# Performance work log

Hardware: AMD Instinct MI355X
Metric: run time of the kernel (lower is better)

## Reference

```python
import jax, jax.numpy as jnp
import numpy as np

B, N, ADA, L, D_OUT, C_T, N_DIS = 8, 2048, 16, 64, 16, 4, 8
H = L // D_OUT  # 4 heads emulated via split/cat on the batch dim


def setup_inputs() -> dict:
    key = jax.random.key(0)
    ks = jax.random.split(key, 12)
    f = lambda i, shape, s=1.0: jax.random.normal(ks[i], shape, dtype=jnp.float32) * s
    return dict(
        c=f(0, (B, N, L)),
        c_condition=f(1, (B, C_T)),
        c_disease=f(2, (B, N_DIS)),
        state=f(3, (B, N, L)),
        emb_normal=f(4, (N, ADA)),                 # nn.Parameter embeddings_normal
        W_q1=f(5, (C_T, L), 0.1), b_q1=jnp.zeros((L,), jnp.float32),
        W_qr1=f(6, (1, L), 0.1),  b_qr1=jnp.zeros((L,), jnp.float32),
        W_q2=f(7, (L, L), 0.1),   b_q2=jnp.zeros((L,), jnp.float32),
        W_qr2=f(8, (L, L), 0.1),  b_qr2=jnp.zeros((L,), jnp.float32),
        Wp_gcn=f(9, (ADA, 2, L, L), 0.1),          # adaptive weight pool (cheb_k=2)
        bp_gcn=f(10, (ADA, L), 0.1),               # adaptive bias pool
    )


def _to_heads(t):
    # torch.cat(torch.split(t, D_OUT, dim=-1), dim=0): [B,N,H*d] -> [H*B,N,d]
    return jnp.concatenate(jnp.split(t, H, axis=-1), axis=0)


def _from_heads(t):
    # inverse: [H*B,N,d] -> [B,N,H*d]
    return jnp.concatenate(jnp.split(t, H, axis=0), axis=-1)


def _anode_gcn(x, E, Wp, bp):
    # adaptive GCN (AGCRN-style AVWGCN): supports=[I, softmax(relu(E E^T))]
    A = jax.nn.softmax(jax.nn.relu(E @ E.T), axis=1)          # [N,N]
    xg = jnp.stack([x, jnp.einsum('nm,bmc->bnc', A, x)], 1)   # [B,2,N,C]
    Wn = jnp.einsum('nd,dkio->nkio', E, Wp)                   # per-node weights
    bn = E @ bp                                               # [N,L]
    return jnp.einsum('bkni,nkio->bno', xg, Wn) + bn


def reference(c, c_condition, c_disease, state, emb_normal,
              W_q1, b_q1, W_qr1, b_qr1, W_q2, b_q2, W_qr2, b_qr2,
              Wp_gcn, bp_gcn):
    # gated query path
    Qt = jax.nn.sigmoid(c_condition[:, None, :] @ W_q1 + b_q1)        # [B,1,L]
    Qt = jnp.tanh((Qt * c) @ W_q2 + b_q2)                             # [B,N,L]
    # disease loop vectorized: sum_n sigmoid(Linear(c_disease[:, n:n+1]))
    qr = jax.nn.sigmoid(c_disease[:, :, None] * W_qr1[0] + b_qr1)     # [B,D,L]
    qr = qr.sum(axis=1, keepdims=True)                                # [B,1,L]
    qr = Qt + jnp.tanh((qr * c) @ W_qr2 + b_qr2)                      # [B,N,L]
    qr_h = _to_heads(qr)  # computed in the original but unused in output

    theta = _to_heads(state)                                          # [HB,N,d]
    ct = jnp.tanh(_anode_gcn(c, emb_normal, Wp_gcn, bp_gcn))          # [B,N,L]
    ct = _to_heads(ct)                                                # [HB,N,d]

    attn = jnp.einsum('bnd,bmd->bnm', theta, theta) / jnp.sqrt(jnp.float32(D_OUT))
    attn = jax.nn.softmax(attn, axis=-1)                              # [HB,N,N]
    x = -jnp.einsum('bnm,bmd->bnd', attn, ct)                         # [HB,N,d]
    return _from_heads(x)                                             # [B,N,L]
```

## Files before the change

### kernel.cpp

```cpp
#include <hip/hip_runtime.h>
#include <hip/hip_bf16.h>

#define NN 2048
#define BB 8
#define LL 64
#define ADA 16
#define DH 16
#define HB 32
#define KT 2048

typedef __attribute__((ext_vector_type(4))) short bf16x4;
typedef __attribute__((ext_vector_type(4))) float f32x4;
typedef __attribute__((ext_vector_type(8))) unsigned short ushort8v;
typedef _Float16 half_t;
typedef __attribute__((ext_vector_type(2))) _Float16 halfx2;
typedef __attribute__((ext_vector_type(4))) _Float16 halfx4;
typedef __attribute__((ext_vector_type(8))) _Float16 halfx8;

#if defined(__HIP_DEVICE_COMPILE__)
#if __has_builtin(__builtin_amdgcn_mfma_f32_16x16x16bf16_1k)
#define MFMA16(a, b, c) __builtin_amdgcn_mfma_f32_16x16x16bf16_1k(a, b, c, 0, 0, 0)
#elif __has_builtin(__builtin_amdgcn_mfma_f32_16x16x16_bf16)
#define MFMA16(a, b, c) __builtin_amdgcn_mfma_f32_16x16x16_bf16(a, b, c, 0, 0, 0)
#else
#error "no 16x16x16 bf16 mfma builtin on device"
#endif
#if __has_builtin(__builtin_amdgcn_mfma_f32_16x16x16f16)
#define MFMA16H(a, b, c) __builtin_amdgcn_mfma_f32_16x16x16f16(a, b, c, 0, 0, 0)
#elif __has_builtin(__builtin_amdgcn_mfma_f32_16x16x16_f16)
#define MFMA16H(a, b, c) __builtin_amdgcn_mfma_f32_16x16x16_f16(a, b, c, 0, 0, 0)
#else
#error "no 16x16x16 f16 mfma builtin on device"
#endif
#if __has_builtin(__builtin_amdgcn_exp2f)
#define EXP2F(x) __builtin_amdgcn_exp2f(x)
#else
#define EXP2F(x) exp2f(x)
#endif
#else
#define MFMA16(a, b, c) (c)
#define MFMA16H(a, b, c) (c)
#define EXP2F(x) exp2f(x)
#endif

__device__ inline halfx2 cvt_pk2(float a, float b) {
#if defined(__HIP_DEVICE_COMPILE__) && __has_builtin(__builtin_amdgcn_cvt_pkrtz)
  auto r = __builtin_amdgcn_cvt_pkrtz(a, b);
  return __builtin_bit_cast(halfx2, r);
#else
  halfx2 r;
  r[0] = (_Float16)a;
  r[1] = (_Float16)b;
  return r;
#endif
}

__device__ inline unsigned short f2bf(float x) {
  __hip_bfloat16 h = __float2bfloat16(x);
  return *reinterpret_cast<unsigned short*>(&h);
}
__device__ inline float tanh_fast(float v) {
  return 1.f - 2.f / (__expf(2.f * v) + 1.f);
}

__global__ __launch_bounds__(256) void k_rowsoftmax(const float* __restrict__ E,
                                                    unsigned short* __restrict__ A16) {
  __shared__ float row[4][NN];
  __shared__ float red[4][256];
  const int n = blockIdx.x * 4;
  const int t = threadIdx.x;
  float4 e[4][4];
#pragma unroll
  for (int r = 0; r < 4; ++r) {
    const float4* Er = (const float4*)(E + (size_t)(n + r) * ADA);
#pragma unroll
    for (int j = 0; j < 4; ++j) e[r][j] = Er[j];
  }
  float l[4] = {0.f, 0.f, 0.f, 0.f};
  for (int m = t; m < NN; m += 256) {
    const float4* Em = (const float4*)(E + (size_t)m * ADA);
    float4 ev[4];
#pragma unroll
    for (int j = 0; j < 4; ++j) ev[j] = Em[j];
#pragma unroll
    for (int r = 0; r < 4; ++r) {
      float s = 0.f;
#pragma unroll
      for (int j = 0; j < 4; ++j) {
        s = fmaf(e[r][j].x, ev[j].x, s);
        s = fmaf(e[r][j].y, ev[j].y, s);
        s = fmaf(e[r][j].z, ev[j].z, s);
        s = fmaf(e[r][j].w, ev[j].w, s);
      }
      float p = __expf(fmaxf(s, 0.f) - 20.f);
      row[r][m] = p;
      l[r] += p;
    }
  }
#pragma unroll
  for (int r = 0; r < 4; ++r) red[r][t] = l[r];
  __syncthreads();
  for (int off = 128; off > 0; off >>= 1) {
    if (t < off) {
#pragma unroll
      for (int r = 0; r < 4; ++r) red[r][t] += red[r][t + off];
    }
    __syncthreads();
  }
  float inv[4];
#pragma unroll
  for (int r = 0; r < 4; ++r) inv[r] = 1.f / red[r][0];
  for (int m = t; m < NN; m += 256) {
#pragma unroll
    for (int r = 0; r < 4; ++r)
      A16[(size_t)(n + r) * NN + m] = f2bf(row[r][m] * inv[r]);
  }
}

__global__ __launch_bounds__(256) void k_prep_c(const float* __restrict__ c,
                                                unsigned short* __restrict__ cT16) {
  __shared__ float ld[64][68];
  const int m0 = blockIdx.x * 64;
  const int b = blockIdx.y;
  const int t = threadIdx.x;
  {
    const int r = t & 63, cq = t >> 6;
    const float* cp = c + ((size_t)b * NN + m0 + r) * LL + cq * 16;
#pragma unroll
    for (int u = 0; u < 4; ++u)
      *(float4*)&ld[r][cq * 16 + 4 * u] = *(const float4*)(cp + 4 * u);
  }
  __syncthreads();
  const int o = t & 63, mq = t >> 6;
  unsigned short outv[16];
#pragma unroll
  for (int v = 0; v < 16; ++v) outv[v] = f2bf(ld[mq * 16 + v][o]);
  unsigned short* op = cT16 + ((size_t)b * LL + o) * NN + m0 + mq * 16;
  *(ushort8v*)op = *(const ushort8v*)&outv[0];
  *(ushort8v*)(op + 8) = *(const ushort8v*)&outv[8];
}

__global__ __launch_bounds__(256) void k_prep_w(const float* __restrict__ Wp,
                                                half_t* __restrict__ WpT) {
  __shared__ float ld[64][68];
  const int k0 = blockIdx.x * 64;
  const int t = threadIdx.x;
  {
    const int r = t & 63, cq = t >> 6;
    const float* wp = Wp + (size_t)(k0 + r) * LL + cq * 16;
#pragma unroll
    for (int u = 0; u < 4; ++u)
      *(float4*)&ld[r][cq * 16 + 4 * u] = *(const float4*)(wp + 4 * u);
  }
  __syncthreads();
  const int o = t & 63, kq = t >> 6;
  halfx8 h0, h1;
#pragma unroll
  for (int v = 0; v < 8; ++v) {
    h0[v] = (half_t)ld[kq * 16 + v][o];
    h1[v] = (half_t)ld[kq * 16 + 8 + v][o];
  }
  half_t* op = WpT + (size_t)o * KT + k0 + kq * 16;
  *(halfx8*)op = h0;
  *(halfx8*)(op + 8) = h1;
}

__global__ __launch_bounds__(256) void k_gemm1(const unsigned short* __restrict__ A16,
                                               const unsigned short* __restrict__ cT16,
                                               float* __restrict__ cg0,
                                               float* __restrict__ cg1) {
  __shared__ unsigned short sA[64][72];
  __shared__ unsigned short sB[64][72];
  const int t = threadIdx.x;
  const int n0 = blockIdx.x * 64;
  const int b = blockIdx.y;
  const int kh = blockIdx.z;
  const int wv = t >> 6, lane = t & 63;
  const int lr = lane & 15, lg = lane >> 4;
  const unsigned short* cb = cT16 + (size_t)b * LL * NN;
  const int sr = t >> 2, sc = (t & 3) * 16;
  f32x4 acc[4];
#pragma unroll
  for (int ot = 0; ot < 4; ++ot) acc[ot] = (f32x4){0.f, 0.f, 0.f, 0.f};

  for (int k0 = kh * (NN / 2); k0 < (kh + 1) * (NN / 2); k0 += 64) {
    __syncthreads();
    {
      const unsigned short* ga = A16 + (size_t)(n0 + sr) * NN + k0 + sc;
      *(ushort8v*)&sA[sr][sc] = *(const ushort8v*)ga;
      *(ushort8v*)&sA[sr][sc + 8] = *(const ushort8v*)(ga + 8);
      const unsigned short* gb = cb + (size_t)sr * NN + k0 + sc;
      *(ushort8v*)&sB[sr][sc] = *(const ushort8v*)gb;
      *(ushort8v*)&sB[sr][sc + 8] = *(const ushort8v*)(gb + 8);
    }
    __syncthreads();
#pragma unroll
    for (int ks = 0; ks < 4; ++ks) {
      bf16x4 a = *(const bf16x4*)&sA[16 * wv + lr][ks * 16 + 4 * lg];
#pragma unroll
      for (int ot = 0; ot < 4; ++ot) {
        bf16x4 bq = *(const bf16x4*)&sB[ot * 16 + lr][ks * 16 + 4 * lg];
        acc[ot] = MFMA16(a, bq, acc[ot]);
      }
    }
  }
  float* outp = (kh ? cg1 : cg0) + ((size_t)b * NN + n0 + 16 * wv) * LL;
#pragma unroll
  for (int ot = 0; ot < 4; ++ot)
#pragma unroll
    for (int reg = 0; reg < 4; ++reg)
      outp[(size_t)(4 * lg + reg) * LL + ot * 16 + lr] = acc[ot][reg];
}

__global__ __launch_bounds__(256) void k_gcn3(const float* __restrict__ E,
                                              const half_t* __restrict__ WpT,
                                              const float* __restrict__ bp,
                                              const float* __restrict__ c,
                                              const float* __restrict__ cg0,
                                              const float* __restrict__ cg1,
                                              float* __restrict__ ctp0,
                                              float* __restrict__ ctp1) {
  __shared__ half_t sW[64][136];
  __shared__ float sE[64][17];
  __shared__ float sbp[16][64];
  const int t = threadIdx.x;
  const int n0 = blockIdx.x * 64;
  const int b = blockIdx.y;
  const int dh = blockIdx.z;
  const int wv = t >> 6, lane = t & 63;
  const int lr = lane & 15, lg = lane >> 4;
  {
    const int r = t >> 2, dq = (t & 3) * 4;
    float4 ev = *(const float4*)(E + (size_t)(n0 + r) * ADA + dq);
    sE[r][dq + 0] = ev.x; sE[r][dq + 1] = ev.y;
    sE[r][dq + 2] = ev.z; sE[r][dq + 3] = ev.w;
    const int bi = t * 4;
    *(float4*)&sbp[bi >> 6][bi & 63] = *(const float4*)(bp + bi);
  }
  float xr[8][4];
  {
    const size_t rbase = ((size_t)b * NN + n0 + 16 * wv + lr) * LL;
#pragma unroll
    for (int q = 0; q < 4; ++q) {
      float4 v = *(const float4*)(c + rbase + q * 16 + 4 * lg);
      xr[q][0] = v.x; xr[q][1] = v.y; xr[q][2] = v.z; xr[q][3] = v.w;
    }
#pragma unroll
    for (int q = 0; q < 4; ++q) {
      float4 a = *(const float4*)(cg0 + rbase + q * 16 + 4 * lg);
      float4 b2 = *(const float4*)(cg1 + rbase + q * 16 + 4 * lg);
      xr[4 + q][0] = a.x + b2.x; xr[4 + q][1] = a.y + b2.y;
      xr[4 + q][2] = a.z + b2.z; xr[4 + q][3] = a.w + b2.w;
    }
  }
  __syncthreads();
  f32x4 acc[4];
  if (dh == 0) {
#pragma unroll
    for (int ot = 0; ot < 4; ++ot) {
      f32x4 s = (f32x4){0.f, 0.f, 0.f, 0.f};
#pragma unroll
      for (int d = 0; d < ADA; ++d) {
        const float bpv = sbp[d][ot * 16 + lr];
#pragma unroll
        for (int reg = 0; reg < 4; ++reg)
          s[reg] = fmaf(sE[16 * wv + 4 * lg + reg][d], bpv, s[reg]);
      }
      acc[ot] = s;
    }
  } else {
#pragma unroll
    for (int ot = 0; ot < 4; ++ot) acc[ot] = (f32x4){0.f, 0.f, 0.f, 0.f};
  }
  const int so = t >> 2, sq = t & 3;
  halfx8 wreg[4];
  {
    const half_t* p = WpT + (size_t)so * KT + (size_t)(dh * 8) * 128;
#pragma unroll
    for (int u = 0; u < 4; ++u) wreg[u] = *(const halfx8*)(p + (sq + 4 * u) * 8);
  }
  for (int dd = 0; dd < 8; ++dd) {
    __syncthreads();
#pragma unroll
    for (int u = 0; u < 4; ++u) *(halfx8*)&sW[so][(sq + 4 * u) * 8] = wreg[u];
    __syncthreads();
    if (dd < 7) {
      const half_t* p = WpT + (size_t)so * KT + (size_t)(dh * 8 + dd + 1) * 128;
#pragma unroll
      for (int u = 0; u < 4; ++u) wreg[u] = *(const halfx8*)(p + (sq + 4 * u) * 8);
    }
    const float e = sE[16 * wv + lr][dh * 8 + dd];
    halfx4 af[8];
#pragma unroll
    for (int kt = 0; kt < 8; ++kt)
#pragma unroll
      for (int j = 0; j < 4; ++j) af[kt][j] = (half_t)(e * xr[kt][j]);
#pragma unroll
    for (int kt = 0; kt < 8; ++kt) {
#pragma unroll
      for (int ot = 0; ot < 4; ++ot) {
        halfx4 bq = *(const halfx4*)&sW[ot * 16 + lr][kt * 16 + 4 * lg];
        acc[ot] = MFMA16H(af[kt], bq, acc[ot]);
      }
    }
  }
  float* op = (dh ? ctp1 : ctp0) + ((size_t)b * NN + n0 + 16 * wv) * LL;
#pragma unroll
  for (int ot = 0; ot < 4; ++ot)
#pragma unroll
    for (int reg = 0; reg < 4; ++reg)
      op[(size_t)(4 * lg + reg) * LL + ot * 16 + lr] = acc[ot][reg];
}

__global__ __launch_bounds__(256) void k_prep(const float* __restrict__ state,
                                              const float* __restrict__ ctp0,
                                              const float* __restrict__ ctp1,
                                              half_t* __restrict__ th16h,
                                              half_t* __restrict__ thq16h,
                                              half_t* __restrict__ vt16h) {
  __shared__ half_t vt[16][68];
  const int hb = blockIdx.x;
  const int h = hb >> 3, b = hb & 7;
  const int n0 = blockIdx.y * 64;
  const int t = threadIdx.x;
  const int r = t >> 2, dq = t & 3;
  const float QS = 0.25f * 1.4426950408889634f;
  const float* sp = state + ((size_t)b * NN + n0 + r) * LL + h * DH + 4 * dq;
  float4 sv = *(const float4*)sp;
  halfx4 tk;
  tk[0] = (half_t)sv.x; tk[1] = (half_t)sv.y; tk[2] = (half_t)sv.z; tk[3] = (half_t)sv.w;
  *(halfx4*)(th16h + ((size_t)hb * NN + n0 + r) * DH + 4 * dq) = tk;
  halfx4 tq;
  tq[0] = (half_t)(QS * sv.x); tq[1] = (half_t)(QS * sv.y);
  tq[2] = (half_t)(QS * sv.z); tq[3] = (half_t)(QS * sv.w);
  *(halfx4*)(thq16h + ((size_t)hb * NN + n0 + r) * DH + 4 * dq) = tq;
  const size_t cidx = ((size_t)b * NN + n0 + r) * LL + h * DH + 4 * dq;
  float4 p0 = *(const float4*)(ctp0 + cidx);
  float4 p1 = *(const float4*)(ctp1 + cidx);
  vt[4 * dq + 0][r] = (half_t)tanh_fast(p0.x + p1.x);
  vt[4 * dq + 1][r] = (half_t)tanh_fast(p0.y + p1.y);
  vt[4 * dq + 2][r] = (half_t)tanh_fast(p0.z + p1.z);
  vt[4 * dq + 3][r] = (half_t)tanh_fast(p0.w + p1.w);
  __syncthreads();
  const int d = t >> 4, mq = t & 15;
  halfx4 o;
  o[0] = vt[d][4 * mq + 0]; o[1] = vt[d][4 * mq + 1];
  o[2] = vt[d][4 * mq + 2]; o[3] = vt[d][4 * mq + 3];
  *(halfx4*)(vt16h + ((size_t)hb * DH + d) * NN + n0 + 4 * mq) = o;
}

__global__ __launch_bounds__(512, 4) void k_attn5(const half_t* __restrict__ th16h,
                                                  const half_t* __restrict__ thq16h,
                                                  const half_t* __restrict__ vt16h,
                                                  float* __restrict__ out) {
  __shared__ float sred[8][8][16][16];
  float* dfl = &sred[0][0][0][0];
  const int hb = blockIdx.x;
  const int h = hb >> 3, b = hb & 7;
  const int wv = threadIdx.x >> 6, lane = threadIdx.x & 63;
  const int q0 = blockIdx.y * 128;
  const int lr = lane & 15, lg = lane >> 4;
  const half_t* th = th16h + (size_t)hb * NN * DH;
  const half_t* thq = thq16h + (size_t)hb * NN * DH;
  const half_t* vrow = vt16h + ((size_t)hb * DH + lr) * NN;
  halfx4 qf[8];
#pragma unroll
  for (int f = 0; f < 8; ++f)
    qf[f] = *(const halfx4*)(thq + (size_t)(q0 + 16 * f + lr) * DH + 4 * lg);
  const float SH = 8.f * 1.4426950408889634f;
  const f32x4 shiftv = {-SH, -SH, -SH, -SH};
  f32x4 acc[8];
  float den[8];
#pragma unroll
  for (int f = 0; f < 8; ++f) { acc[f] = (f32x4){0.f, 0.f, 0.f, 0.f}; den[f] = 0.f; }

  const int mb = wv * (NN / 8);
  halfx4 kf = *(const halfx4*)(th + (size_t)(mb + lr) * DH + 4 * lg);
  halfx4 vf = *(const halfx4*)(vrow + mb + 4 * lg);
  for (int mt = 0; mt < NN / 128; ++mt) {
    halfx4 kf_n = kf, vf_n = vf;
    if (mt < NN / 128 - 1) {
      const int mn = mb + (mt + 1) * 16;
      kf_n = *(const halfx4*)(th + (size_t)(mn + lr) * DH + 4 * lg);
      vf_n = *(const halfx4*)(vrow + mn + 4 * lg);
    }
#pragma unroll
    for (int f = 0; f < 8; ++f) {
      f32x4 s = MFMA16H(kf, qf[f], shiftv);
      float p0 = EXP2F(s[0]), p1 = EXP2F(s[1]), p2 = EXP2F(s[2]), p3 = EXP2F(s[3]);
      den[f] += (p0 + p1) + (p2 + p3);
      halfx2 lo = cvt_pk2(p0, p1), hi = cvt_pk2(p2, p3);
      halfx4 pf;
      pf[0] = lo[0]; pf[1] = lo[1]; pf[2] = hi[0]; pf[3] = hi[1];
      acc[f] = MFMA16H(pf, vf, acc[f]);
    }
    kf = kf_n; vf = vf_n;
  }
#pragma unroll
  for (int f = 0; f < 8; ++f) {
    den[f] += __shfl_xor(den[f], 16);
    den[f] += __shfl_xor(den[f], 32);
  }
  if (lane < 16) {
#pragma unroll
    for (int f = 0; f < 8; ++f) dfl[(wv * 8 + f) * 16 + lane] = den[f];
  }
  __syncthreads();
  const int t = threadIdx.x;
  const int fo = t >> 6, ro = (t >> 2) & 15, duo = (t & 3) * 4;
  float ds = 0.f;
#pragma unroll
  for (int w = 0; w < 8; ++w) ds += dfl[(w * 8 + fo) * 16 + ro];
  __syncthreads();
#pragma unroll
  for (int f = 0; f < 8; ++f) {
#pragma unroll
    for (int reg = 0; reg < 4; ++reg) sred[wv][f][4 * lg + reg][lr] = acc[f][reg];
  }
  __syncthreads();
  float4 ns = make_float4(0.f, 0.f, 0.f, 0.f);
#pragma unroll
  for (int w = 0; w < 8; ++w) {
    float4 v = *(const float4*)&sred[w][fo][ro][duo];
    ns.x += v.x; ns.y += v.y; ns.z += v.z; ns.w += v.w;
  }
  const float inv = -1.f / ds;
  float4 o = make_float4(ns.x * inv, ns.y * inv, ns.z * inv, ns.w * inv);
  *(float4*)(out + ((size_t)b * NN + q0 + 16 * fo + ro) * LL + h * DH + duo) = o;
}

extern "C" void kernel_launch(void* const* d_in, const int* in_sizes, int n_in,
                              void* d_out, int out_size, void* d_ws, size_t ws_size,
                              hipStream_t stream) {
  const float* c = (const float*)d_in[0];
  const float* state = (const float*)d_in[3];
  const float* E = (const float*)d_in[4];
  const float* Wp = (const float*)d_in[13];
  const float* bp = (const float*)d_in[14];
  float* out = (float*)d_out;

  unsigned short* A16 = (unsigned short*)d_ws;
  unsigned short* cT16 = A16 + (size_t)NN * NN;
  half_t* WpT = (half_t*)(cT16 + (size_t)BB * LL * NN);
  float* cg0 = (float*)(WpT + (size_t)LL * KT);
  float* cg1 = cg0 + (size_t)BB * NN * LL;
  float* ctp0 = cg1 + (size_t)BB * NN * LL;
  float* ctp1 = ctp0 + (size_t)BB * NN * LL;
  half_t* th16h = (half_t*)(ctp1 + (size_t)BB * NN * LL);
  half_t* thq16h = th16h + (size_t)HB * NN * DH;
  half_t* vt16h = thq16h + (size_t)HB * NN * DH;

  k_rowsoftmax<<<NN / 4, 256, 0, stream>>>(E, A16);
  k_prep_c<<<dim3(NN / 64, BB), 256, 0, stream>>>(c, cT16);
  k_prep_w<<<KT / 64, 256, 0, stream>>>(Wp, WpT);
  k_gemm1<<<dim3(NN / 64, BB, 2), 256, 0, stream>>>(A16, cT16, cg0, cg1);
  k_gcn3<<<dim3(NN / 64, BB, 2), 256, 0, stream>>>(E, WpT, bp, c, cg0, cg1, ctp0, ctp1);
  k_prep<<<dim3(HB, NN / 64), 256, 0, stream>>>(state, ctp0, ctp1, th16h, thq16h, vt16h);
  k_attn5<<<dim3(HB, NN / 128), 512, 0, stream>>>(th16h, thq16h, vt16h, out);
}
```

Before: 76.41 us.

## Merge prep kernels into one launch and fuse tanh/value transpose into GCN

Merges the row-softmax, c-transpose, weight-transpose and state/theta conversion into a single multi-role kernel dispatched on block index, cutting launches. The GCN kernel now splits over output halves instead of the ADA dimension, so each block covers all 16 embedding dims for 32 outputs. It applies tanh and writes the transposed fp16 value tensor directly, which removes the ctp0/ctp1 fp32 intermediates and the separate prep kernel. In exchange each GCN block does a longer serial loop with more barriers, and the merged prep kernel has uneven block roles.

```diff
diff --git a/kernel.cpp b/kernel.cpp
--- a/kernel.cpp
+++ b/kernel.cpp
@@ -63,106 +63,131 @@
   return 1.f - 2.f / (__expf(2.f * v) + 1.f);
 }
 
-__global__ __launch_bounds__(256) void k_rowsoftmax(const float* __restrict__ E,
-                                                    unsigned short* __restrict__ A16) {
-  __shared__ float row[4][NN];
-  __shared__ float red[4][256];
-  const int n = blockIdx.x * 4;
+__global__ __launch_bounds__(256) void k_preps(const float* __restrict__ E,
+                                               const float* __restrict__ c,
+                                               const float* __restrict__ state,
+                                               const float* __restrict__ Wp,
+                                               unsigned short* __restrict__ A16,
+                                               unsigned short* __restrict__ cT16,
+                                               half_t* __restrict__ WpT,
+                                               half_t* __restrict__ th16h,
+                                               half_t* __restrict__ thq16h) {
+  __shared__ float sbuf[4 * 2304];
+  const int id = blockIdx.x;
   const int t = threadIdx.x;
-  float4 e[4][4];
-#pragma unroll
-  for (int r = 0; r < 4; ++r) {
-    const float4* Er = (const float4*)(E + (size_t)(n + r) * ADA);
-#pragma unroll
-    for (int j = 0; j < 4; ++j) e[r][j] = Er[j];
-  }
-  float l[4] = {0.f, 0.f, 0.f, 0.f};
-  for (int m = t; m < NN; m += 256) {
-    const float4* Em = (const float4*)(E + (size_t)m * ADA);
-    float4 ev[4];
-#pragma unroll
-    for (int j = 0; j < 4; ++j) ev[j] = Em[j];
+  if (id < 512) {
+    float(*row)[NN] = (float(*)[NN])sbuf;
+    float(*red)[256] = (float(*)[256])(sbuf + 4 * NN);
+    const int n = id * 4;
+    float4 e[4][4];
 #pragma unroll
     for (int r = 0; r < 4; ++r) {
-      float s = 0.f;
-#pragma unroll
-      for (int j = 0; j < 4; ++j) {
-        s = fmaf(e[r][j].x, ev[j].x, s);
-        s = fmaf(e[r][j].y, ev[j].y, s);
-        s = fmaf(e[r][j].z, ev[j].z, s);
-        s = fmaf(e[r][j].w, ev[j].w, s);
+      const float4* Er = (const float4*)(E + (size_t)(n + r) * ADA);
+#pragma unroll
+      for (int j = 0; j < 4; ++j) e[r][j] = Er[j];
+    }
+    float l[4] = {0.f, 0.f, 0.f, 0.f};
+    for (int m = t; m < NN; m += 256) {
+      const float4* Em = (const float4*)(E + (size_t)m * ADA);
+      float4 ev[4];
+#pragma unroll
+      for (int j = 0; j < 4; ++j) ev[j] = Em[j];
+#pragma unroll
+      for (int r = 0; r < 4; ++r) {
+        float s = 0.f;
+#pragma unroll
+        for (int j = 0; j < 4; ++j) {
+          s = fmaf(e[r][j].x, ev[j].x, s);
+          s = fmaf(e[r][j].y, ev[j].y, s);
+          s = fmaf(e[r][j].z, ev[j].z, s);
+          s = fmaf(e[r][j].w, ev[j].w, s);
+        }
+        float p = __expf(fmaxf(s, 0.f) - 20.f);
+        row[r][m] = p;
+        l[r] += p;
       }
-      float p = __expf(fmaxf(s, 0.f) - 20.f);
-      row[r][m] = p;
-      l[r] += p;
-    }
-  }
-#pragma unroll
-  for (int r = 0; r < 4; ++r) red[r][t] = l[r];
-  __syncthreads();
-  for (int off = 128; off > 0; off >>= 1) {
-    if (t < off) {
-#pragma unroll
-      for (int r = 0; r < 4; ++r) red[r][t] += red[r][t + off];
-    }
-    __syncthreads();
-  }
-  float inv[4];
-#pragma unroll
-  for (int r = 0; r < 4; ++r) inv[r] = 1.f / red[r][0];
-  for (int m = t; m < NN; m += 256) {
-#pragma unroll
-    for (int r = 0; r < 4; ++r)
-      A16[(size_t)(n + r) * NN + m] = f2bf(row[r][m] * inv[r]);
-  }
-}
-
-__global__ __launch_bounds__(256) void k_prep_c(const float* __restrict__ c,
-                                                unsigned short* __restrict__ cT16) {
-  __shared__ float ld[64][68];
-  const int m0 = blockIdx.x * 64;
-  const int b = blockIdx.y;
-  const int t = threadIdx.x;
-  {
-    const int r = t & 63, cq = t >> 6;
-    const float* cp = c + ((size_t)b * NN + m0 + r) * LL + cq * 16;
-#pragma unroll
-    for (int u = 0; u < 4; ++u)
-      *(float4*)&ld[r][cq * 16 + 4 * u] = *(const float4*)(cp + 4 * u);
-  }
-  __syncthreads();
-  const int o = t & 63, mq = t >> 6;
-  unsigned short outv[16];
-#pragma unroll
-  for (int v = 0; v < 16; ++v) outv[v] = f2bf(ld[mq * 16 + v][o]);
-  unsigned short* op = cT16 + ((size_t)b * LL + o) * NN + m0 + mq * 16;
-  *(ushort8v*)op = *(const ushort8v*)&outv[0];
-  *(ushort8v*)(op + 8) = *(const ushort8v*)&outv[8];
-}
-
-__global__ __launch_bounds__(256) void k_prep_w(const float* __restrict__ Wp,
-                                                half_t* __restrict__ WpT) {
-  __shared__ float ld[64][68];
-  const int k0 = blockIdx.x * 64;
-  const int t = threadIdx.x;
-  {
-    const int r = t & 63, cq = t >> 6;
-    const float* wp = Wp + (size_t)(k0 + r) * LL + cq * 16;
-#pragma unroll
-    for (int u = 0; u < 4; ++u)
-      *(float4*)&ld[r][cq * 16 + 4 * u] = *(const float4*)(wp + 4 * u);
-  }
-  __syncthreads();
-  const int o = t & 63, kq = t >> 6;
-  halfx8 h0, h1;
-#pragma unroll
-  for (int v = 0; v < 8; ++v) {
-    h0[v] = (half_t)ld[kq * 16 + v][o];
-    h1[v] = (half_t)ld[kq * 16 + 8 + v][o];
-  }
-  half_t* op = WpT + (size_t)o * KT + k0 + kq * 16;
-  *(halfx8*)op = h0;
-  *(halfx8*)(op + 8) = h1;
+    }
+#pragma unroll
+    for (int r = 0; r < 4; ++r) red[r][t] = l[r];
+    __syncthreads();
+    for (int off = 128; off > 0; off >>= 1) {
+      if (t < off) {
+#pragma unroll
+        for (int r = 0; r < 4; ++r) red[r][t] += red[r][t + off];
+      }
+      __syncthreads();
+    }
+    float inv[4];
+#pragma unroll
+    for (int r = 0; r < 4; ++r) inv[r] = 1.f / red[r][0];
+    for (int m = t; m < NN; m += 256) {
+#pragma unroll
+      for (int r = 0; r < 4; ++r)
+        A16[(size_t)(n + r) * NN + m] = f2bf(row[r][m] * inv[r]);
+    }
+  } else if (id < 768) {
+    float(*ld)[68] = (float(*)[68])sbuf;
+    const int idx = id - 512;
+    const int m0 = (idx & 31) * 64;
+    const int b = idx >> 5;
+    {
+      const int r = t & 63, cq = t >> 6;
+      const float* cp = c + ((size_t)b * NN + m0 + r) * LL + cq * 16;
+#pragma unroll
+      for (int u = 0; u < 4; ++u)
+        *(float4*)&ld[r][cq * 16 + 4 * u] = *(const float4*)(cp + 4 * u);
+    }
+    __syncthreads();
+    const int o = t & 63, mq = t >> 6;
+    unsigned short outv[16];
+#pragma unroll
+    for (int v = 0; v < 16; ++v) outv[v] = f2bf(ld[mq * 16 + v][o]);
+    unsigned short* op = cT16 + ((size_t)b * LL + o) * NN + m0 + mq * 16;
+    *(ushort8v*)op = *(const ushort8v*)&outv[0];
+    *(ushort8v*)(op + 8) = *(const ushort8v*)&outv[8];
+  } else if (id < 800) {
+    float(*ld)[68] = (float(*)[68])sbuf;
+    const int k0 = (id - 768) * 64;
+    {
+      const int r = t & 63, cq = t >> 6;
+      const float* wp = Wp + (size_t)(k0 + r) * LL + cq * 16;
+#pragma unroll
+      for (int u = 0; u < 4; ++u)
+        *(float4*)&ld[r][cq * 16 + 4 * u] = *(const float4*)(wp + 4 * u);
+    }
+    __syncthreads();
+    const int o = t & 63, kq = t >> 6;
+    halfx8 h0, h1;
+#pragma unroll
+    for (int v = 0; v < 8; ++v) {
+      h0[v] = (half_t)ld[kq * 16 + v][o];
+      h1[v] = (half_t)ld[kq * 16 + 8 + v][o];
+    }
+    half_t* op = WpT + (size_t)o * KT + k0 + kq * 16;
+    *(halfx8*)op = h0;
+    *(halfx8*)(op + 8) = h1;
+  } else {
+    const int idx = id - 800;
+    const int n0 = (idx & 31) * 64;
+    const int b = idx >> 5;
+    const int r = t >> 2, h = t & 3;
+    const float QS = 0.25f * 1.4426950408889634f;
+    const float* sp = state + ((size_t)b * NN + n0 + r) * LL + h * DH;
+    half_t tk[16], tq[16];
+#pragma unroll
+    for (int u = 0; u < 4; ++u) {
+      float4 sv = *(const float4*)(sp + 4 * u);
+      tk[4 * u + 0] = (half_t)sv.x; tk[4 * u + 1] = (half_t)sv.y;
+      tk[4 * u + 2] = (half_t)sv.z; tk[4 * u + 3] = (half_t)sv.w;
+      tq[4 * u + 0] = (half_t)(QS * sv.x); tq[4 * u + 1] = (half_t)(QS * sv.y);
+      tq[4 * u + 2] = (half_t)(QS * sv.z); tq[4 * u + 3] = (half_t)(QS * sv.w);
+    }
+    const size_t base = ((size_t)(h * 8 + b) * NN + n0 + r) * DH;
+    *(halfx8*)(th16h + base) = *(const halfx8*)&tk[0];
+    *(halfx8*)(th16h + base + 8) = *(const halfx8*)&tk[8];
+    *(halfx8*)(thq16h + base) = *(const halfx8*)&tq[0];
+    *(halfx8*)(thq16h + base + 8) = *(const halfx8*)&tq[8];
+  }
 }
 
 __global__ __launch_bounds__(256) void k_gemm1(const unsigned short* __restrict__ A16,
@@ -212,21 +237,20 @@
       outp[(size_t)(4 * lg + reg) * LL + ot * 16 + lr] = acc[ot][reg];
 }
 
-__global__ __launch_bounds__(256) void k_gcn3(const float* __restrict__ E,
+__global__ __launch_bounds__(256) void k_gcn4(const float* __restrict__ E,
                                               const half_t* __restrict__ WpT,
                                               const float* __restrict__ bp,
                                               const float* __restrict__ c,
                                               const float* __restrict__ cg0,
                                               const float* __restrict__ cg1,
-                                              float* __restrict__ ctp0,
-                                              float* __restrict__ ctp1) {
-  __shared__ half_t sW[64][136];
+                                              half_t* __restrict__ vt16h) {
+  __shared__ half_t sW[32][136];
   __shared__ float sE[64][17];
-  __shared__ float sbp[16][64];
+  __shared__ float sbp[16][32];
   const int t = threadIdx.x;
   const int n0 = blockIdx.x * 64;
   const int b = blockIdx.y;
-  const int dh = blockIdx.z;
+  const int oh = blockIdx.z;
   const int wv = t >> 6, lane = t & 63;
   const int lr = lane & 15, lg = lane >> 4;
   {
@@ -234,8 +258,10 @@
     float4 ev = *(const float4*)(E + (size_t)(n0 + r) * ADA + dq);
     sE[r][dq + 0] = ev.x; sE[r][dq + 1] = ev.y;
     sE[r][dq + 2] = ev.z; sE[r][dq + 3] = ev.w;
-    const int bi = t * 4;
-    *(float4*)&sbp[bi >> 6][bi & 63] = *(const float4*)(bp + bi);
+    const int d = t >> 4, o2 = (t & 15) * 2;
+    float2 bv = *(const float2*)(bp + d * LL + oh * 32 + o2);
+    sbp[d][o2] = bv.x;
+    sbp[d][o2 + 1] = bv.y;
   }
   float xr[8][4];
   {
@@ -254,99 +280,59 @@
     }
   }
   __syncthreads();
-  f32x4 acc[4];
-  if (dh == 0) {
-#pragma unroll
-    for (int ot = 0; ot < 4; ++ot) {
-      f32x4 s = (f32x4){0.f, 0.f, 0.f, 0.f};
-#pragma unroll
-      for (int d = 0; d < ADA; ++d) {
-        const float bpv = sbp[d][ot * 16 + lr];
-#pragma unroll
-        for (int reg = 0; reg < 4; ++reg)
-          s[reg] = fmaf(sE[16 * wv + 4 * lg + reg][d], bpv, s[reg]);
+  f32x4 acc[2];
+#pragma unroll
+  for (int ot2 = 0; ot2 < 2; ++ot2) {
+    f32x4 s = (f32x4){0.f, 0.f, 0.f, 0.f};
+#pragma unroll
+    for (int d = 0; d < ADA; ++d) {
+      const float bpv = sbp[d][ot2 * 16 + lr];
+#pragma unroll
+      for (int reg = 0; reg < 4; ++reg)
+        s[reg] = fmaf(sE[16 * wv + 4 * lg + reg][d], bpv, s[reg]);
+    }
+    acc[ot2] = s;
+  }
+  const int so = t >> 3, sq = t & 7;
+  halfx8 wreg[2];
+  {
+    const half_t* p = WpT + (size_t)(oh * 32 + so) * KT + sq * 16;
+    wreg[0] = *(const halfx8*)p;
+    wreg[1] = *(const halfx8*)(p + 8);
+  }
+  for (int dd = 0; dd < ADA; ++dd) {
+    __syncthreads();
+    *(halfx8*)&sW[so][sq * 16] = wreg[0];
+    *(halfx8*)&sW[so][sq * 16 + 8] = wreg[1];
+    __syncthreads();
+    if (dd < ADA - 1) {
+      const half_t* p = WpT + (size_t)(oh * 32 + so) * KT + (dd + 1) * 128 + sq * 16;
+      wreg[0] = *(const halfx8*)p;
+      wreg[1] = *(const halfx8*)(p + 8);
+    }
+    const float e = sE[16 * wv + lr][dd];
+    halfx4 af[8];
+#pragma unroll
+    for (int kt = 0; kt < 8; ++kt)
+#pragma unroll
+      for (int j = 0; j < 4; ++j) af[kt][j] = (half_t)(e * xr[kt][j]);
+#pragma unroll
+    for (int kt = 0; kt < 8; ++kt) {
+#pragma unroll
+      for (int ot2 = 0; ot2 < 2; ++ot2) {
+        halfx4 bq = *(const halfx4*)&sW[ot2 * 16 + lr][kt * 16 + 4 * lg];
+        acc[ot2] = MFMA16H(af[kt], bq, acc[ot2]);
       }
-      acc[ot] = s;
-    }
-  } else {
-#pragma unroll
-    for (int ot = 0; ot < 4; ++ot) acc[ot] = (f32x4){0.f, 0.f, 0.f, 0.f};
-  }
-  const int so = t >> 2, sq = t & 3;
-  halfx8 wreg[4];
-  {
-    const half_t* p = WpT + (size_t)so * KT + (size_t)(dh * 8) * 128;
-#pragma unroll
-    for (int u = 0; u < 4; ++u) wreg[u] = *(const halfx8*)(p + (sq + 4 * u) * 8);
-  }
-  for (int dd = 0; dd < 8; ++dd) {
-    __syncthreads();
-#pragma unroll
-    for (int u = 0; u < 4; ++u) *(halfx8*)&sW[so][(sq + 4 * u) * 8] = wreg[u];
-    __syncthreads();
-    if (dd < 7) {
-      const half_t* p = WpT + (size_t)so * KT + (size_t)(dh * 8 + dd + 1) * 128;
-#pragma unroll
-      for (int u = 0; u < 4; ++u) wreg[u] = *(const halfx8*)(p + (sq + 4 * u) * 8);
-    }
-    const float e = sE[16 * wv + lr][dh * 8 + dd];
-    halfx4 af[8];
-#pragma unroll
-    for (int kt = 0; kt < 8; ++kt)
-#pragma unroll
-      for (int j = 0; j < 4; ++j) af[kt][j] = (half_t)(e * xr[kt][j]);
-#pragma unroll
-    for (int kt = 0; kt < 8; ++kt) {
-#pragma unroll
-      for (int ot = 0; ot < 4; ++ot) {
-        halfx4 bq = *(const halfx4*)&sW[ot * 16 + lr][kt * 16 + 4 * lg];
-        acc[ot] = MFMA16H(af[kt], bq, acc[ot]);
-      }
-    }
-  }
-  float* op = (dh ? ctp1 : ctp0) + ((size_t)b * NN + n0 + 16 * wv) * LL;
-#pragma unroll
-  for (int ot = 0; ot < 4; ++ot)
-#pragma unroll
-    for (int reg = 0; reg < 4; ++reg)
-      op[(size_t)(4 * lg + reg) * LL + ot * 16 + lr] = acc[ot][reg];
-}
-
-__global__ __launch_bounds__(256) void k_prep(const float* __restrict__ state,
-                                              const float* __restrict__ ctp0,
-                                              const float* __restrict__ ctp1,
-                                              half_t* __restrict__ th16h,
-                                              half_t* __restrict__ thq16h,
-                                              half_t* __restrict__ vt16h) {
-  __shared__ half_t vt[16][68];
-  const int hb = blockIdx.x;
-  const int h = hb >> 3, b = hb & 7;
-  const int n0 = blockIdx.y * 64;
-  const int t = threadIdx.x;
-  const int r = t >> 2, dq = t & 3;
-  const float QS = 0.25f * 1.4426950408889634f;
-  const float* sp = state + ((size_t)b * NN + n0 + r) * LL + h * DH + 4 * dq;
-  float4 sv = *(const float4*)sp;
-  halfx4 tk;
-  tk[0] = (half_t)sv.x; tk[1] = (half_t)sv.y; tk[2] = (half_t)sv.z; tk[3] = (half_t)sv.w;
-  *(halfx4*)(th16h + ((size_t)hb * NN + n0 + r) * DH + 4 * dq) = tk;
-  halfx4 tq;
-  tq[0] = (half_t)(QS * sv.x); tq[1] = (half_t)(QS * sv.y);
-  tq[2] = (half_t)(QS * sv.z); tq[3] = (half_t)(QS * sv.w);
-  *(halfx4*)(thq16h + ((size_t)hb * NN + n0 + r) * DH + 4 * dq) = tq;
-  const size_t cidx = ((size_t)b * NN + n0 + r) * LL + h * DH + 4 * dq;
-  float4 p0 = *(const float4*)(ctp0 + cidx);
-  float4 p1 = *(const float4*)(ctp1 + cidx);
-  vt[4 * dq + 0][r] = (half_t)tanh_fast(p0.x + p1.x);
-  vt[4 * dq + 1][r] = (half_t)tanh_fast(p0.y + p1.y);
-  vt[4 * dq + 2][r] = (half_t)tanh_fast(p0.z + p1.z);
-  vt[4 * dq + 3][r] = (half_t)tanh_fast(p0.w + p1.w);
-  __syncthreads();
-  const int d = t >> 4, mq = t & 15;
-  halfx4 o;
-  o[0] = vt[d][4 * mq + 0]; o[1] = vt[d][4 * mq + 1];
-  o[2] = vt[d][4 * mq + 2]; o[3] = vt[d][4 * mq + 3];
-  *(halfx4*)(vt16h + ((size_t)hb * DH + d) * NN + n0 + 4 * mq) = o;
+    }
+  }
+#pragma unroll
+  for (int ot2 = 0; ot2 < 2; ++ot2) {
+    const int h = oh * 2 + ot2;
+    halfx4 o4;
+#pragma unroll
+    for (int reg = 0; reg < 4; ++reg) o4[reg] = (half_t)tanh_fast(acc[ot2][reg]);
+    *(halfx4*)(vt16h + ((size_t)(h * 8 + b) * DH + lr) * NN + n0 + 16 * wv + 4 * lg) = o4;
+  }
 }
 
 __global__ __launch_bounds__(512, 4) void k_attn5(const half_t* __restrict__ th16h,
@@ -444,17 +430,12 @@
   half_t* WpT = (half_t*)(cT16 + (size_t)BB * LL * NN);
   float* cg0 = (float*)(WpT + (size_t)LL * KT);
   float* cg1 = cg0 + (size_t)BB * NN * LL;
-  float* ctp0 = cg1 + (size_t)BB * NN * LL;
-  float* ctp1 = ctp0 + (size_t)BB * NN * LL;
-  half_t* th16h = (half_t*)(ctp1 + (size_t)BB * NN * LL);
+  half_t* th16h = (half_t*)(cg1 + (size_t)BB * NN * LL);
   half_t* thq16h = th16h + (size_t)HB * NN * DH;
   half_t* vt16h = thq16h + (size_t)HB * NN * DH;
 
-  k_rowsoftmax<<<NN / 4, 256, 0, stream>>>(E, A16);
-  k_prep_c<<<dim3(NN / 64, BB), 256, 0, stream>>>(c, cT16);
-  k_prep_w<<<KT / 64, 256, 0, stream>>>(Wp, WpT);
+  k_preps<<<1056, 256, 0, stream>>>(E, c, state, Wp, A16, cT16, WpT, th16h, thq16h);
   k_gemm1<<<dim3(NN / 64, BB, 2), 256, 0, stream>>>(A16, cT16, cg0, cg1);
-  k_gcn3<<<dim3(NN / 64, BB, 2), 256, 0, stream>>>(E, WpT, bp, c, cg0, cg1, ctp0, ctp1);
-  k_prep<<<dim3(HB, NN / 64), 256, 0, stream>>>(state, ctp0, ctp1, th16h, thq16h, vt16h);
+  k_gcn4<<<dim3(NN / 64, BB, 2), 256, 0, stream>>>(E, WpT, bp, c, cg0, cg1, vt16h);
   k_attn5<<<dim3(HB, NN / 128), 512, 0, stream>>>(th16h, thq16h, vt16h, out);
 }
```

New measurement: 72.78 us. -4.7%, faster.
